# Optimization experiments

Measured on AMD Instinct MI355X. Metric: run time of the kernel, lower is better.

The kernel has to match this reference:

```python
import jax, jax.numpy as jnp
import numpy as np

T = 8192          # sequence length
E = 1024          # embedding_dim
H = 1024          # hidden_dim
HD = H // 2       # per-direction hidden
K = 34            # tagset size
START, STOP = 32, 33
NEG = -10000.0


def setup_inputs() -> dict:
    key = jax.random.key(0)
    ks = jax.random.split(key, 16)
    s = 1.0 / np.sqrt(HD)  # torch LSTM/Linear init scale
    u = lambda k, shp, sc: jax.random.uniform(k, shp, jnp.float32, -sc, sc)
    inp = {
        "sentence": jax.random.normal(ks[0], (T, E), jnp.float32),
        "h0": jax.random.normal(ks[1], (2, HD), jnp.float32),
        "c0": jax.random.normal(ks[2], (2, HD), jnp.float32),
        "w_ih_f": u(ks[3], (4 * HD, E), s),
        "w_hh_f": u(ks[4], (4 * HD, HD), s),
        "b_ih_f": u(ks[5], (4 * HD,), s),
        "b_hh_f": u(ks[6], (4 * HD,), s),
        "w_ih_b": u(ks[7], (4 * HD, E), s),
        "w_hh_b": u(ks[8], (4 * HD, HD), s),
        "b_ih_b": u(ks[9], (4 * HD,), s),
        "b_hh_b": u(ks[10], (4 * HD,), s),
        "w_out": u(ks[11], (K, H), 1.0 / np.sqrt(H)),
        "b_out": u(ks[12], (K,), 1.0 / np.sqrt(H)),
    }
    trans = jax.random.normal(ks[13], (K, K), jnp.float32)
    trans = trans.at[START, :].set(NEG).at[:, STOP].set(NEG)
    inp["transitions"] = trans
    return inp


def _lstm_dir(x_proj, h0, c0, w_hh, reverse):
    # x_proj: [T, 4*HD] precomputed input projection (+ both biases)
    def step(carry, xp):
        h, c = carry
        g = xp + h @ w_hh.T
        i, f, gg, o = jnp.split(g, 4)
        i, f, o = jax.nn.sigmoid(i), jax.nn.sigmoid(f), jax.nn.sigmoid(o)
        c = f * c + i * jnp.tanh(gg)
        h = o * jnp.tanh(c)
        return (h, c), h
    _, hs = jax.lax.scan(step, (h0, c0), x_proj, reverse=reverse)
    return hs  # [T, HD]


def reference(sentence, h0, c0, w_ih_f, w_hh_f, b_ih_f, b_hh_f,
              w_ih_b, w_hh_b, b_ih_b, b_hh_b, w_out, b_out, transitions):
    # BiLSTM encoder (dropout is identity at inference)
    xp_f = sentence @ w_ih_f.T + (b_ih_f + b_hh_f)
    xp_b = sentence @ w_ih_b.T + (b_ih_b + b_hh_b)
    hs_f = _lstm_dir(xp_f, h0[0], c0[0], w_hh_f, reverse=False)
    hs_b = _lstm_dir(xp_b, h0[1], c0[1], w_hh_b, reverse=True)
    lstm_out = jnp.concatenate([hs_f, hs_b], axis=-1)        # [T, H]
    feats = lstm_out @ w_out.T + b_out                        # [T, K]

    # Viterbi decode: scores[next, prev] = fv[prev] + transitions[next, prev]
    fv0 = jnp.full((K,), NEG, jnp.float32).at[START].set(0.0)

    def vit_step(fv, feat):
        scores = fv[None, :] + transitions                    # [K, K]
        bp = jnp.argmax(scores, axis=1)                       # best prev per next
        fv_new = jnp.max(scores, axis=1) + feat
        return fv_new, bp

    fv, bps = jax.lax.scan(vit_step, fv0, feats)              # bps: [T, K]
    terminal = fv + transitions[STOP]
    best_last = jnp.argmax(terminal)
    path_score = terminal[best_last]

    def back_step(tag, bp_t):
        return bp_t[tag], tag

    _, best_path = jax.lax.scan(back_step, best_last, bps, reverse=True)  # [T]
    return path_score, best_path, sentence
```

## Files before the change

### kernel.cpp

```cpp
#include <hip/hip_runtime.h>
#include <hip/hip_bf16.h>

typedef float v4f __attribute__((ext_vector_type(4)));
typedef int   v4i __attribute__((ext_vector_type(4)));

#define T_LEN 8192
#define E_DIM 1024
#define HD    512
#define G4    2048
#define K_TAGS 34

#define XP_OFF      0ull
#define HS_OFF      134217728ull
#define FEATS_OFF   167772160ull
#define BP_OFF      168886272ull
#define FLAGS_OFF   169164800ull
#define BEST_OFF    169165824ull

#define BM 128
#define BN 128
#define BKK 16

__global__ __launch_bounds__(256) void xp_gemm(
    const float* __restrict__ A, const float* __restrict__ Wf, const float* __restrict__ Wb,
    const float* __restrict__ bihf, const float* __restrict__ bhhf,
    const float* __restrict__ bihb, const float* __restrict__ bhhb,
    float* __restrict__ xp)
{
  __shared__ __align__(16) float a_lds[BKK][BM + 4];
  __shared__ __align__(16) float b_lds[BKK][BN + 4];
  const int dir = blockIdx.z;
  const float* W   = dir ? Wb : Wf;
  const float* bih = dir ? bihb : bihf;
  const float* bhh = dir ? bhhb : bhhf;
  const int tid = threadIdx.x;
  const int srow = tid >> 1, sh = (tid & 1) * 8;
  const int tx = tid & 15, ty = tid >> 4;
  const size_t arow = (size_t)(blockIdx.x * BM + srow) * E_DIM;
  const size_t brow = (size_t)(blockIdx.y * BN + srow) * E_DIM;
  float acc[8][8];
  #pragma unroll
  for (int i = 0; i < 8; ++i)
    #pragma unroll
    for (int j = 0; j < 8; ++j) acc[i][j] = 0.f;

  for (int k0 = 0; k0 < E_DIM; k0 += BKK) {
    v4f a0 = *(const v4f*)(A + arow + k0 + sh);
    v4f a1 = *(const v4f*)(A + arow + k0 + sh + 4);
    v4f b0 = *(const v4f*)(W + brow + k0 + sh);
    v4f b1 = *(const v4f*)(W + brow + k0 + sh + 4);
    __syncthreads();
    #pragma unroll
    for (int j = 0; j < 4; ++j) {
      a_lds[sh + j][srow]     = a0[j];
      a_lds[sh + 4 + j][srow] = a1[j];
      b_lds[sh + j][srow]     = b0[j];
      b_lds[sh + 4 + j][srow] = b1[j];
    }
    __syncthreads();
    #pragma unroll
    for (int kk = 0; kk < BKK; ++kk) {
      v4f av0 = *(const v4f*)&a_lds[kk][ty * 8];
      v4f av1 = *(const v4f*)&a_lds[kk][ty * 8 + 4];
      v4f bv0 = *(const v4f*)&b_lds[kk][tx * 4];
      v4f bv1 = *(const v4f*)&b_lds[kk][64 + tx * 4];
      float av[8] = {av0[0],av0[1],av0[2],av0[3],av1[0],av1[1],av1[2],av1[3]};
      float bv[8] = {bv0[0],bv0[1],bv0[2],bv0[3],bv1[0],bv1[1],bv1[2],bv1[3]};
      #pragma unroll
      for (int i = 0; i < 8; ++i)
        #pragma unroll
        for (int j = 0; j < 8; ++j) acc[i][j] = fmaf(av[i], bv[j], acc[i][j]);
    }
  }
  const int gm  = blockIdx.x * BM + ty * 8;
  const int gnl = blockIdx.y * BN + tx * 4;
  const int gnh = gnl + 64;
  float bias[8];
  #pragma unroll
  for (int j = 0; j < 4; ++j) bias[j]     = bih[gnl + j] + bhh[gnl + j];
  #pragma unroll
  for (int j = 0; j < 4; ++j) bias[4 + j] = bih[gnh + j] + bhh[gnh + j];
  float* outp = xp + ((size_t)dir * T_LEN) * G4;
  #pragma unroll
  for (int i = 0; i < 8; ++i) {
    v4f o0 = {acc[i][0]+bias[0], acc[i][1]+bias[1], acc[i][2]+bias[2], acc[i][3]+bias[3]};
    v4f o1 = {acc[i][4]+bias[4], acc[i][5]+bias[5], acc[i][6]+bias[6], acc[i][7]+bias[7]};
    *(v4f*)(outp + (size_t)(gm + i) * G4 + gnl) = o0;
    *(v4f*)(outp + (size_t)(gm + i) * G4 + gnh) = o1;
  }
}

__device__ __forceinline__ float row16_sum(float x) {
  x += __int_as_float(__builtin_amdgcn_update_dpp(0, __float_as_int(x), 0x111, 0xf, 0xf, true));
  x += __int_as_float(__builtin_amdgcn_update_dpp(0, __float_as_int(x), 0x112, 0xf, 0xf, true));
  x += __int_as_float(__builtin_amdgcn_update_dpp(0, __float_as_int(x), 0x114, 0xf, 0xf, true));
  x += __int_as_float(__builtin_amdgcn_update_dpp(0, __float_as_int(x), 0x118, 0xf, 0xf, true));
  return x;
}

__device__ __forceinline__ float sigmoidf_(float x) { return 1.f / (1.f + expf(-x)); }

__global__ __launch_bounds__(1024) void lstm_kernel(
    const float* __restrict__ h0, const float* __restrict__ c0,
    const float* __restrict__ whhf, const float* __restrict__ whhb,
    const float* __restrict__ xp, float* __restrict__ hs)
{
  const int b = blockIdx.x;
  const int dir = b >> 5, bb = b & 31;
  const int tid = threadIdx.x;
  const int w = tid >> 6, L = tid & 63;
  const float* whh = dir ? whhb : whhf;
  const float* xpd = xp + (size_t)dir * T_LEN * G4;
  float* hsd = hs + (size_t)dir * T_LEN * HD;
  __shared__ __align__(16) float red2[16][4][4];
  __shared__ float xpl[2][64];
  __shared__ float gl[4][16];

  float wreg[4][8];
  #pragma unroll
  for (int j = 0; j < 4; ++j) {
    int r = 4 * w + j;
    int grow = (r >> 4) * HD + bb * 16 + (r & 15);
    const float* p = whh + (size_t)grow * HD + 8 * L;
    v4f q0 = *(const v4f*)p;
    v4f q1 = *(const v4f*)(p + 4);
    #pragma unroll
    for (int kk = 0; kk < 4; ++kk) { wreg[j][kk] = q0[kk]; wreg[j][4 + kk] = q1[kk]; }
  }
  float cst = (tid < 16) ? c0[dir * HD + bb * 16 + tid] : 0.f;
  if (tid >= 64 && tid < 128) {
    int r = tid - 64;
    int col = (r >> 4) * HD + bb * 16 + (r & 15);
    int t0 = dir ? (T_LEN - 1) : 0;
    xpl[0][r] = xpd[(size_t)t0 * G4 + col];
  }
  __syncthreads();

  for (int s = 0; s < T_LEN; ++s) {
    const int t = dir ? (T_LEN - 1 - s) : s;
    __syncthreads();

    float hr[8];
    if (s == 0) {
      const float* hp = h0 + dir * HD + 8 * L;
      v4f h0v = *(const v4f*)hp;
      v4f h1v = *(const v4f*)(hp + 4);
      #pragma unroll
      for (int kk = 0; kk < 4; ++kk) { hr[kk] = h0v[kk]; hr[4 + kk] = h1v[kk]; }
    } else {
      const int tp = dir ? (t + 1) : (t - 1);
      const float* hp = hsd + (size_t)tp * HD + 8 * L;
      v4i ia, ib;
      do {
        asm volatile("global_load_dwordx4 %0, %2, off sc0 sc1\n"
                     "global_load_dwordx4 %1, %2, off offset:16 sc0 sc1\n"
                     "s_waitcnt vmcnt(0)"
                     : "=&v"(ia), "=&v"(ib) : "v"(hp) : "memory");
      } while (((ia[0] == -1) | (ia[1] == -1) | (ia[2] == -1) | (ia[3] == -1) |
                (ib[0] == -1) | (ib[1] == -1) | (ib[2] == -1) | (ib[3] == -1)) != 0);
      #pragma unroll
      for (int kk = 0; kk < 4; ++kk) {
        hr[kk]     = __int_as_float(ia[kk]);
        hr[4 + kk] = __int_as_float(ib[kk]);
      }
    }

    float a4[4];
    #pragma unroll
    for (int j = 0; j < 4; ++j) {
      float a = 0.f;
      #pragma unroll
      for (int kk = 0; kk < 8; ++kk) a = fmaf(wreg[j][kk], hr[kk], a);
      a4[j] = row16_sum(a);
    }
    if ((L & 15) == 15) {
      int q = L >> 4;
      v4f rv = {a4[0], a4[1], a4[2], a4[3]};
      *(v4f*)&red2[w][q][0] = rv;
    }
    __syncthreads();

    if (tid < 64) {
      const int u = tid & 15, g = tid >> 4;
      const int r = g * 16 + u;
      const int ww = r >> 2, j = r & 3;
      const float sum = red2[ww][0][j] + red2[ww][1][j] + red2[ww][2][j] + red2[ww][3][j]
                      + xpl[s & 1][r];
      const float gv = (g == 2) ? tanhf(sum) : sigmoidf_(sum);
      gl[g][u] = gv;
      asm volatile("s_waitcnt lgkmcnt(0)" ::: "memory");
      if (tid < 16) {
        const float ig = gl[0][u];
        const float fg = gl[1][u];
        const float gg = gl[2][u];
        const float og = gl[3][u];
        cst = fg * cst + ig * gg;
        const float hval = og * tanhf(cst);
        float* hp = hsd + (size_t)t * HD + bb * 16 + u;
        asm volatile("global_store_dword %0, %1, off sc0 sc1" :: "v"(hp), "v"(hval) : "memory");
      }
    } else if (tid >= 64 && tid < 128 && s + 1 < T_LEN) {
      const int r = tid - 64;
      const int col = (r >> 4) * HD + bb * 16 + (r & 15);
      const int tn = dir ? (t - 1) : (t + 1);
      xpl[(s + 1) & 1][r] = xpd[(size_t)tn * G4 + col];
    }
  }
}

__global__ __launch_bounds__(256) void feats_kernel(
    const float* __restrict__ hs, const float* __restrict__ wout,
    const float* __restrict__ bout, float* __restrict__ feats)
{
  __shared__ __align__(16) float xs[32][132];
  __shared__ __align__(16) float wl[34][132];
  const int tid = threadIdx.x;
  const int t0 = blockIdx.x * 32;
  const int m = tid & 31, ng = tid >> 5;
  float acc[5] = {0.f, 0.f, 0.f, 0.f, 0.f};
  for (int cc = 0; cc < 8; ++cc) {
    const int d = cc >> 2;
    const int c0 = (cc & 3) * 128;
    const float* hsrc = hs + (size_t)d * T_LEN * HD;
    const int wcol = d * HD + c0;
    __syncthreads();
    {
      const int row = tid >> 3, seg = tid & 7;
      const float* src = hsrc + (size_t)(t0 + row) * HD + c0 + seg * 16;
      #pragma unroll
      for (int i = 0; i < 4; ++i) {
        v4f v = *(const v4f*)(src + i * 4);
        *(v4f*)&xs[row][seg * 16 + i * 4] = v;
      }
    }
    for (int i = tid; i < 34 * 32; i += 256) {
      const int r = i >> 5, q = i & 31;
      v4f v = *(const v4f*)(wout + (size_t)r * E_DIM + wcol + q * 4);
      *(v4f*)&wl[r][q * 4] = v;
    }
    __syncthreads();
    for (int kq = 0; kq < 32; ++kq) {
      v4f xv = *(const v4f*)&xs[m][kq * 4];
      #pragma unroll
      for (int sl = 0; sl < 5; ++sl) {
        const int n = ng + sl * 8;
        if (n < K_TAGS) {
          v4f wv = *(const v4f*)&wl[n][kq * 4];
          acc[sl] = fmaf(xv[0], wv[0], acc[sl]);
          acc[sl] = fmaf(xv[1], wv[1], acc[sl]);
          acc[sl] = fmaf(xv[2], wv[2], acc[sl]);
          acc[sl] = fmaf(xv[3], wv[3], acc[sl]);
        }
      }
    }
  }
  #pragma unroll
  for (int sl = 0; sl < 5; ++sl) {
    const int n = ng + sl * 8;
    if (n < K_TAGS) feats[(size_t)(t0 + m) * K_TAGS + n] = acc[sl] + bout[n];
  }
}

__global__ __launch_bounds__(64) void viterbi_kernel(
    const float* __restrict__ feats, const float* __restrict__ trans,
    float* __restrict__ d_out, int* __restrict__ bestlast, unsigned char* __restrict__ bp)
{
  const int L = threadIdx.x;
  const int n = (L < K_TAGS) ? L : 0;
  const bool act = (L < K_TAGS);
  float tr[K_TAGS];
  #pragma unroll
  for (int p = 0; p < K_TAGS; ++p) tr[p] = trans[n * K_TAGS + p];
  const float tstop = trans[33 * K_TAGS + n];
  __shared__ float fvs[K_TAGS];
  if (act) fvs[n] = (n == 32) ? 0.f : -10000.f;
  __syncthreads();
  float feat_next = feats[n];
  float fvreg = 0.f;
  for (int t = 0; t < T_LEN; ++t) {
    const float feat = feat_next;
    if (t + 1 < T_LEN) feat_next = feats[(size_t)(t + 1) * K_TAGS + n];
    float best = -3.4e38f; int bi = 0;
    #pragma unroll
    for (int p = 0; p < K_TAGS; ++p) {
      const float v = fvs[p] + tr[p];
      const bool gt = v > best;
      bi = gt ? p : bi;
      best = gt ? v : best;
    }
    fvreg = best + feat;
    if (act) bp[(size_t)t * K_TAGS + n] = (unsigned char)bi;
    __syncthreads();
    if (act) fvs[n] = fvreg;
    __syncthreads();
  }
  if (act) fvs[n] = fvreg + tstop;
  __syncthreads();
  if (L == 0) {
    float best = -3.4e38f; int bi = 0;
    for (int k = 0; k < K_TAGS; ++k) {
      const float v = fvs[k];
      if (v > best) { best = v; bi = k; }
    }
    d_out[0] = best;
    *bestlast = bi;
  }
}

__global__ __launch_bounds__(1024) void backtrace_kernel(
    const unsigned char* __restrict__ bp, const int* __restrict__ bestlast,
    float* __restrict__ d_out)
{
  __shared__ unsigned char exitl[128 * K_TAGS];
  __shared__ unsigned char entl[128];
  const int tid = threadIdx.x;
  for (int W = tid; W < 128 * K_TAGS; W += 1024) {
    const int c = W / K_TAGS;
    int tg = W % K_TAGS;
    for (int t = c * 64 + 63; t >= c * 64; --t) tg = bp[(size_t)t * K_TAGS + tg];
    exitl[W] = (unsigned char)tg;
  }
  __syncthreads();
  if (tid == 0) {
    int tag = *bestlast;
    entl[127] = (unsigned char)tag;
    for (int c = 127; c >= 1; --c) {
      tag = exitl[c * K_TAGS + tag];
      entl[c - 1] = (unsigned char)tag;
    }
  }
  __syncthreads();
  if (tid < 128) {
    const int c = tid;
    int tg = entl[c];
    for (int t = c * 64 + 63; t >= c * 64; --t) {
      d_out[1 + t] = (float)tg;
      tg = bp[(size_t)t * K_TAGS + tg];
    }
  }
}

extern "C" void kernel_launch(void* const* d_in, const int* in_sizes, int n_in,
                              void* d_out, int out_size, void* d_ws, size_t ws_size,
                              hipStream_t stream)
{
  const float* sent = (const float*)d_in[0];
  const float* h0   = (const float*)d_in[1];
  const float* c0   = (const float*)d_in[2];
  const float* wihf = (const float*)d_in[3];
  const float* whhf = (const float*)d_in[4];
  const float* bihf = (const float*)d_in[5];
  const float* bhhf = (const float*)d_in[6];
  const float* wihb = (const float*)d_in[7];
  const float* whhb = (const float*)d_in[8];
  const float* bihb = (const float*)d_in[9];
  const float* bhhb = (const float*)d_in[10];
  const float* wout = (const float*)d_in[11];
  const float* bout = (const float*)d_in[12];
  const float* trans = (const float*)d_in[13];

  float* out = (float*)d_out;
  char* ws = (char*)d_ws;
  float* xp    = (float*)(ws + XP_OFF);
  float* hs    = (float*)(ws + HS_OFF);
  float* feats = (float*)(ws + FEATS_OFF);
  unsigned char* bp = (unsigned char*)(ws + BP_OFF);
  int* bestlast = (int*)(ws + BEST_OFF);

  hipMemsetAsync(hs, 0xFF, (size_t)2 * T_LEN * HD * sizeof(float), stream);

  hipMemcpyAsync(out + 1 + T_LEN, sent, (size_t)T_LEN * E_DIM * sizeof(float),
                 hipMemcpyDeviceToDevice, stream);

  dim3 g1(T_LEN / BM, G4 / BN, 2);
  xp_gemm<<<g1, 256, 0, stream>>>(sent, wihf, wihb, bihf, bhhf, bihb, bhhb, xp);

  lstm_kernel<<<64, 1024, 0, stream>>>(h0, c0, whhf, whhb, xp, hs);

  feats_kernel<<<T_LEN / 32, 256, 0, stream>>>(hs, wout, bout, feats);

  viterbi_kernel<<<1, 64, 0, stream>>>(feats, trans, out, bestlast, bp);

  backtrace_kernel<<<1, 1024, 0, stream>>>(bp, bestlast, out);
}
```

Measured before the change: 20.27 ms.

## Use single-wave LSTM blocks and a barrier-free tree-argmax Viterbi

The recurrent LSTM kernel is re-split from 64 blocks of 1024 threads into 512 single-wavefront blocks. Each wave owns two hidden units, all 8 gate rows, and does the whole reduction with DPP and cross-lane shuffles. This removes the LDS staging and two __syncthreads per timestep from the serial critical path, at the cost of more waves spinning on the global hidden-state flags. The Viterbi kernel also drops its block barriers, since it runs as one wave, and replaces the linear argmax scan with a tree reduction that keeps the lowest index on ties.

After: 25.36 ms. +25.1%, slower.

```diff
diff --git a/kernel.cpp b/kernel.cpp
--- a/kernel.cpp
+++ b/kernel.cpp
@@ -14,7 +14,6 @@
 #define HS_OFF      134217728ull
 #define FEATS_OFF   167772160ull
 #define BP_OFF      168886272ull
-#define FLAGS_OFF   169164800ull
 #define BEST_OFF    169165824ull
 
 #define BM 128
@@ -100,53 +99,46 @@
 
 __device__ __forceinline__ float sigmoidf_(float x) { return 1.f / (1.f + expf(-x)); }
 
-__global__ __launch_bounds__(1024) void lstm_kernel(
+__global__ __launch_bounds__(64) void lstm_kernel(
     const float* __restrict__ h0, const float* __restrict__ c0,
     const float* __restrict__ whhf, const float* __restrict__ whhb,
     const float* __restrict__ xp, float* __restrict__ hs)
 {
   const int b = blockIdx.x;
-  const int dir = b >> 5, bb = b & 31;
-  const int tid = threadIdx.x;
-  const int w = tid >> 6, L = tid & 63;
+  const int dir = b >> 8, bu = b & 255;
+  const int L = threadIdx.x;
   const float* whh = dir ? whhb : whhf;
   const float* xpd = xp + (size_t)dir * T_LEN * G4;
   float* hsd = hs + (size_t)dir * T_LEN * HD;
-  __shared__ __align__(16) float red2[16][4][4];
-  __shared__ float xpl[2][64];
-  __shared__ float gl[4][16];
-
-  float wreg[4][8];
-  #pragma unroll
-  for (int j = 0; j < 4; ++j) {
-    int r = 4 * w + j;
-    int grow = (r >> 4) * HD + bb * 16 + (r & 15);
+
+  float wreg[8][8];
+  #pragma unroll
+  for (int r = 0; r < 8; ++r) {
+    const int grow = (r >> 1) * HD + 2 * bu + (r & 1);
     const float* p = whh + (size_t)grow * HD + 8 * L;
     v4f q0 = *(const v4f*)p;
     v4f q1 = *(const v4f*)(p + 4);
     #pragma unroll
-    for (int kk = 0; kk < 4; ++kk) { wreg[j][kk] = q0[kk]; wreg[j][4 + kk] = q1[kk]; }
-  }
-  float cst = (tid < 16) ? c0[dir * HD + bb * 16 + tid] : 0.f;
-  if (tid >= 64 && tid < 128) {
-    int r = tid - 64;
-    int col = (r >> 4) * HD + bb * 16 + (r & 15);
-    int t0 = dir ? (T_LEN - 1) : 0;
-    xpl[0][r] = xpd[(size_t)t0 * G4 + col];
-  }
-  __syncthreads();
+    for (int kk = 0; kk < 4; ++kk) { wreg[r][kk] = q0[kk]; wreg[r][4 + kk] = q1[kk]; }
+  }
+  float cst = (L < 2) ? c0[dir * HD + 2 * bu + L] : 0.f;
+  const int growL = (L < 8) ? ((L >> 1) * HD + 2 * bu + (L & 1)) : 0;
+  float xpc = 0.f;
+  {
+    const int t0 = dir ? (T_LEN - 1) : 0;
+    if (L < 8) xpc = xpd[(size_t)t0 * G4 + growL];
+  }
 
   for (int s = 0; s < T_LEN; ++s) {
     const int t = dir ? (T_LEN - 1 - s) : s;
-    __syncthreads();
 
     float hr[8];
     if (s == 0) {
       const float* hp = h0 + dir * HD + 8 * L;
-      v4f h0v = *(const v4f*)hp;
-      v4f h1v = *(const v4f*)(hp + 4);
-      #pragma unroll
-      for (int kk = 0; kk < 4; ++kk) { hr[kk] = h0v[kk]; hr[4 + kk] = h1v[kk]; }
+      v4f a = *(const v4f*)hp;
+      v4f bq = *(const v4f*)(hp + 4);
+      #pragma unroll
+      for (int kk = 0; kk < 4; ++kk) { hr[kk] = a[kk]; hr[4 + kk] = bq[kk]; }
     } else {
       const int tp = dir ? (t + 1) : (t - 1);
       const float* hp = hsd + (size_t)tp * HD + 8 * L;
@@ -165,45 +157,51 @@
       }
     }
 
-    float a4[4];
-    #pragma unroll
-    for (int j = 0; j < 4; ++j) {
+    const float xpv = xpc;
+    if (L < 8 && s + 1 < T_LEN) {
+      const int tn = dir ? (t - 1) : (t + 1);
+      xpc = xpd[(size_t)tn * G4 + growL];
+    }
+
+    float acc[8];
+    #pragma unroll
+    for (int r = 0; r < 8; ++r) {
       float a = 0.f;
       #pragma unroll
-      for (int kk = 0; kk < 8; ++kk) a = fmaf(wreg[j][kk], hr[kk], a);
-      a4[j] = row16_sum(a);
-    }
-    if ((L & 15) == 15) {
-      int q = L >> 4;
-      v4f rv = {a4[0], a4[1], a4[2], a4[3]};
-      *(v4f*)&red2[w][q][0] = rv;
-    }
-    __syncthreads();
-
-    if (tid < 64) {
-      const int u = tid & 15, g = tid >> 4;
-      const int r = g * 16 + u;
-      const int ww = r >> 2, j = r & 3;
-      const float sum = red2[ww][0][j] + red2[ww][1][j] + red2[ww][2][j] + red2[ww][3][j]
-                      + xpl[s & 1][r];
-      const float gv = (g == 2) ? tanhf(sum) : sigmoidf_(sum);
-      gl[g][u] = gv;
-      asm volatile("s_waitcnt lgkmcnt(0)" ::: "memory");
-      if (tid < 16) {
-        const float ig = gl[0][u];
-        const float fg = gl[1][u];
-        const float gg = gl[2][u];
-        const float og = gl[3][u];
-        cst = fg * cst + ig * gg;
-        const float hval = og * tanhf(cst);
-        float* hp = hsd + (size_t)t * HD + bb * 16 + u;
-        asm volatile("global_store_dword %0, %1, off sc0 sc1" :: "v"(hp), "v"(hval) : "memory");
-      }
-    } else if (tid >= 64 && tid < 128 && s + 1 < T_LEN) {
-      const int r = tid - 64;
-      const int col = (r >> 4) * HD + bb * 16 + (r & 15);
-      const int tn = dir ? (t - 1) : (t + 1);
-      xpl[(s + 1) & 1][r] = xpd[(size_t)tn * G4 + col];
+      for (int kk = 0; kk < 8; ++kk) a = fmaf(wreg[r][kk], hr[kk], a);
+      acc[r] = row16_sum(a);
+    }
+    float tot[8];
+    #pragma unroll
+    for (int r = 0; r < 8; ++r) {
+      const float s0 = __shfl(acc[r], 15);
+      const float s1 = __shfl(acc[r], 31);
+      const float s2 = __shfl(acc[r], 47);
+      const float s3 = __shfl(acc[r], 63);
+      tot[r] = ((s0 + s1) + s2) + s3;
+    }
+    const float m01 = (L & 1) ? tot[1] : tot[0];
+    const float m23 = (L & 1) ? tot[3] : tot[2];
+    const float m45 = (L & 1) ? tot[5] : tot[4];
+    const float m67 = (L & 1) ? tot[7] : tot[6];
+    const float m03 = (L & 2) ? m23 : m01;
+    const float m47 = (L & 2) ? m67 : m45;
+    const float mine = (L & 4) ? m47 : m03;
+
+    float gv = 0.f;
+    if (L < 8) {
+      const float sum = mine + xpv;
+      gv = ((L >> 1) == 2) ? tanhf(sum) : sigmoidf_(sum);
+    }
+    const float ig = __shfl(gv, (L & 1));
+    const float fg = __shfl(gv, (L & 1) + 2);
+    const float gg = __shfl(gv, (L & 1) + 4);
+    const float og = __shfl(gv, (L & 1) + 6);
+    if (L < 2) {
+      cst = fg * cst + ig * gg;
+      const float hval = og * tanhf(cst);
+      float* hp = hsd + (size_t)t * HD + 2 * bu + L;
+      asm volatile("global_store_dword %0, %1, off sc0 sc1" :: "v"(hp), "v"(hval) : "memory");
     }
   }
 }
@@ -274,28 +272,36 @@
   const float tstop = trans[33 * K_TAGS + n];
   __shared__ float fvs[K_TAGS];
   if (act) fvs[n] = (n == 32) ? 0.f : -10000.f;
-  __syncthreads();
+  asm volatile("s_waitcnt lgkmcnt(0)" ::: "memory");
+  __builtin_amdgcn_sched_barrier(0);
+
   float feat_next = feats[n];
   float fvreg = 0.f;
   for (int t = 0; t < T_LEN; ++t) {
     const float feat = feat_next;
     if (t + 1 < T_LEN) feat_next = feats[(size_t)(t + 1) * K_TAGS + n];
-    float best = -3.4e38f; int bi = 0;
-    #pragma unroll
-    for (int p = 0; p < K_TAGS; ++p) {
-      const float v = fvs[p] + tr[p];
-      const bool gt = v > best;
-      bi = gt ? p : bi;
-      best = gt ? v : best;
-    }
-    fvreg = best + feat;
-    if (act) bp[(size_t)t * K_TAGS + n] = (unsigned char)bi;
-    __syncthreads();
-    if (act) fvs[n] = fvreg;
-    __syncthreads();
+    float val[K_TAGS];
+    int   idx[K_TAGS];
+    #pragma unroll
+    for (int p = 0; p < K_TAGS; ++p) { val[p] = fvs[p] + tr[p]; idx[p] = p; }
+    #pragma unroll
+    for (int st = 1; st < K_TAGS; st <<= 1) {
+      #pragma unroll
+      for (int i = 0; i + st < K_TAGS; i += 2 * st) {
+        if (val[i + st] > val[i]) { val[i] = val[i + st]; idx[i] = idx[i + st]; }
+      }
+    }
+    fvreg = val[0] + feat;
+    if (act) {
+      bp[(size_t)t * K_TAGS + n] = (unsigned char)idx[0];
+      fvs[n] = fvreg;
+    }
+    asm volatile("s_waitcnt lgkmcnt(0)" ::: "memory");
+    __builtin_amdgcn_sched_barrier(0);
   }
   if (act) fvs[n] = fvreg + tstop;
-  __syncthreads();
+  asm volatile("s_waitcnt lgkmcnt(0)" ::: "memory");
+  __builtin_amdgcn_sched_barrier(0);
   if (L == 0) {
     float best = -3.4e38f; int bi = 0;
     for (int k = 0; k < K_TAGS; ++k) {
@@ -375,7 +381,7 @@
   dim3 g1(T_LEN / BM, G4 / BN, 2);
   xp_gemm<<<g1, 256, 0, stream>>>(sent, wihf, wihb, bihf, bhhf, bihb, bhhb, xp);
 
-  lstm_kernel<<<64, 1024, 0, stream>>>(h0, c0, whhf, whhb, xp, hs);
+  lstm_kernel<<<512, 64, 0, stream>>>(h0, c0, whhf, whhb, xp, hs);
 
   feats_kernel<<<T_LEN / 32, 256, 0, stream>>>(hs, wout, bout, feats);
 
```

## Broadcast LSTM hidden state via LDS and drop Viterbi block barriers

Applied to the files above, without the earlier changes.

In the LSTM kernel, only wave 0 now spin-polls the previous hidden state from global memory and stages it in shared memory, so the other 15 waves stop issuing redundant polling loads. The existing barrier is moved after the staging step. In the single-wave Viterbi kernel, __syncthreads is replaced with lgkmcnt waits plus sched barriers, and the sequential argmax becomes a tree reduction with a shorter dependency chain. The Viterbi change relies on the block being exactly one wavefront. The tree reduction may also break ties differently from first-max argmax semantics.

After: 19.80 ms. -2.3%, faster.

```diff
diff --git a/kernel.cpp b/kernel.cpp
--- a/kernel.cpp
+++ b/kernel.cpp
@@ -14,7 +14,6 @@
 #define HS_OFF      134217728ull
 #define FEATS_OFF   167772160ull
 #define BP_OFF      168886272ull
-#define FLAGS_OFF   169164800ull
 #define BEST_OFF    169165824ull
 
 #define BM 128
@@ -113,6 +112,7 @@
   const float* xpd = xp + (size_t)dir * T_LEN * G4;
   float* hsd = hs + (size_t)dir * T_LEN * HD;
   __shared__ __align__(16) float red2[16][4][4];
+  __shared__ __align__(16) float hl[HD];
   __shared__ float xpl[2][64];
   __shared__ float gl[4][16];
 
@@ -138,33 +138,37 @@
 
   for (int s = 0; s < T_LEN; ++s) {
     const int t = dir ? (T_LEN - 1 - s) : s;
-    __syncthreads();
-
-    float hr[8];
-    if (s == 0) {
-      const float* hp = h0 + dir * HD + 8 * L;
-      v4f h0v = *(const v4f*)hp;
-      v4f h1v = *(const v4f*)(hp + 4);
-      #pragma unroll
-      for (int kk = 0; kk < 4; ++kk) { hr[kk] = h0v[kk]; hr[4 + kk] = h1v[kk]; }
-    } else {
-      const int tp = dir ? (t + 1) : (t - 1);
-      const float* hp = hsd + (size_t)tp * HD + 8 * L;
-      v4i ia, ib;
-      do {
-        asm volatile("global_load_dwordx4 %0, %2, off sc0 sc1\n"
-                     "global_load_dwordx4 %1, %2, off offset:16 sc0 sc1\n"
-                     "s_waitcnt vmcnt(0)"
-                     : "=&v"(ia), "=&v"(ib) : "v"(hp) : "memory");
-      } while (((ia[0] == -1) | (ia[1] == -1) | (ia[2] == -1) | (ia[3] == -1) |
-                (ib[0] == -1) | (ib[1] == -1) | (ib[2] == -1) | (ib[3] == -1)) != 0);
-      #pragma unroll
-      for (int kk = 0; kk < 4; ++kk) {
-        hr[kk]     = __int_as_float(ia[kk]);
-        hr[4 + kk] = __int_as_float(ib[kk]);
-      }
-    }
-
+
+    if (w == 0) {
+      if (s == 0) {
+        const float* hp = h0 + dir * HD + 8 * L;
+        v4f a = *(const v4f*)hp;
+        v4f bq = *(const v4f*)(hp + 4);
+        *(v4f*)&hl[8 * L]     = a;
+        *(v4f*)&hl[8 * L + 4] = bq;
+      } else {
+        const int tp = dir ? (t + 1) : (t - 1);
+        const float* hp = hsd + (size_t)tp * HD + 8 * L;
+        v4i ia, ib;
+        do {
+          asm volatile("global_load_dwordx4 %0, %2, off sc0 sc1\n"
+                       "global_load_dwordx4 %1, %2, off offset:16 sc0 sc1\n"
+                       "s_waitcnt vmcnt(0)"
+                       : "=&v"(ia), "=&v"(ib) : "v"(hp) : "memory");
+        } while (((ia[0] == -1) | (ia[1] == -1) | (ia[2] == -1) | (ia[3] == -1) |
+                  (ib[0] == -1) | (ib[1] == -1) | (ib[2] == -1) | (ib[3] == -1)) != 0);
+        v4f fa, fb;
+        #pragma unroll
+        for (int kk = 0; kk < 4; ++kk) { fa[kk] = __int_as_float(ia[kk]); fb[kk] = __int_as_float(ib[kk]); }
+        *(v4f*)&hl[8 * L]     = fa;
+        *(v4f*)&hl[8 * L + 4] = fb;
+      }
+    }
+    __syncthreads();
+
+    v4f h0v = *(const v4f*)&hl[8 * L];
+    v4f h1v = *(const v4f*)&hl[8 * L + 4];
+    float hr[8] = {h0v[0], h0v[1], h0v[2], h0v[3], h1v[0], h1v[1], h1v[2], h1v[3]};
     float a4[4];
     #pragma unroll
     for (int j = 0; j < 4; ++j) {
@@ -274,28 +278,36 @@
   const float tstop = trans[33 * K_TAGS + n];
   __shared__ float fvs[K_TAGS];
   if (act) fvs[n] = (n == 32) ? 0.f : -10000.f;
-  __syncthreads();
+  asm volatile("s_waitcnt lgkmcnt(0)" ::: "memory");
+  __builtin_amdgcn_sched_barrier(0);
+
   float feat_next = feats[n];
   float fvreg = 0.f;
   for (int t = 0; t < T_LEN; ++t) {
     const float feat = feat_next;
     if (t + 1 < T_LEN) feat_next = feats[(size_t)(t + 1) * K_TAGS + n];
-    float best = -3.4e38f; int bi = 0;
-    #pragma unroll
-    for (int p = 0; p < K_TAGS; ++p) {
-      const float v = fvs[p] + tr[p];
-      const bool gt = v > best;
-      bi = gt ? p : bi;
-      best = gt ? v : best;
-    }
-    fvreg = best + feat;
-    if (act) bp[(size_t)t * K_TAGS + n] = (unsigned char)bi;
-    __syncthreads();
-    if (act) fvs[n] = fvreg;
-    __syncthreads();
+    float val[K_TAGS];
+    int   idx[K_TAGS];
+    #pragma unroll
+    for (int p = 0; p < K_TAGS; ++p) { val[p] = fvs[p] + tr[p]; idx[p] = p; }
+    #pragma unroll
+    for (int st = 1; st < K_TAGS; st <<= 1) {
+      #pragma unroll
+      for (int i = 0; i + st < K_TAGS; i += 2 * st) {
+        if (val[i + st] > val[i]) { val[i] = val[i + st]; idx[i] = idx[i + st]; }
+      }
+    }
+    fvreg = val[0] + feat;
+    if (act) {
+      bp[(size_t)t * K_TAGS + n] = (unsigned char)idx[0];
+      fvs[n] = fvreg;
+    }
+    asm volatile("s_waitcnt lgkmcnt(0)" ::: "memory");
+    __builtin_amdgcn_sched_barrier(0);
   }
   if (act) fvs[n] = fvreg + tstop;
-  __syncthreads();
+  asm volatile("s_waitcnt lgkmcnt(0)" ::: "memory");
+  __builtin_amdgcn_sched_barrier(0);
   if (L == 0) {
     float best = -3.4e38f; int bi = 0;
     for (int k = 0; k < K_TAGS; ++k) {
```
